# Kernel tuning notes

Hardware: AMD Instinct MI355X
Metric: run time of the kernel (lower is better)

The kernel has to match this reference:

```python
import jax, jax.numpy as jnp
import numpy as np

CACHE_LEN = 1024
EPS = 1e-5

def layer_norm(x, g, b):
    m = jnp.mean(x, axis=-1, keepdims=True)
    var = jnp.mean(jnp.square(x - m), axis=-1, keepdims=True)
    return (x - m) * jax.lax.rsqrt(var + EPS) * g + b

def setup_inputs() -> dict:
    key = jax.random.key(0)
    ks = jax.random.split(key, 16)
    B, Lq, Lk, D_IN, D_OUT = 4, 4096, 5119, 512, 512
    s = 1.0 / np.sqrt(D_IN)
    return {
        "q": jax.random.normal(ks[0], (B, Lq, D_IN), jnp.float32),
        "k": jax.random.normal(ks[1], (B, Lk, D_IN), jnp.float32),
        "v": jax.random.normal(ks[2], (B, Lk, D_IN), jnp.float32),
        "gq": jnp.ones((D_IN,), jnp.float32),
        "bq": jnp.zeros((D_IN,), jnp.float32),
        "gk": jnp.ones((D_IN,), jnp.float32),
        "bk": jnp.zeros((D_IN,), jnp.float32),
        "gv": jnp.ones((D_IN,), jnp.float32),
        "bv": jnp.zeros((D_IN,), jnp.float32),
        "Wq": jax.random.uniform(ks[3], (D_IN, D_OUT), jnp.float32, -s, s),
        "bwq": jax.random.uniform(ks[4], (D_OUT,), jnp.float32, -s, s),
        "Wk": jax.random.uniform(ks[5], (D_IN, D_OUT), jnp.float32, -s, s),
        "bwk": jax.random.uniform(ks[6], (D_OUT,), jnp.float32, -s, s),
        "Wv": jax.random.uniform(ks[7], (D_IN, D_OUT), jnp.float32, -s, s),
        "bwv": jax.random.uniform(ks[8], (D_OUT,), jnp.float32, -s, s),
    }

def reference(q, k, v, gq, bq, gk, bk, gv, bv, Wq, bwq, Wk, bwk, Wv, bwv):
    B, Lq, _ = q.shape
    Lk = k.shape[1]
    qp = layer_norm(q, gq, bq) @ Wq + bwq            # [B,Lq,Do]
    kp = layer_norm(k, gk, bk) @ Wk + bwk            # [B,Lk,Do]
    vp = layer_norm(v, gv, bv) @ Wv + bwv            # [B,Lk,Do]
    kv = jax.nn.relu(kp) * vp                         # [B,Lk,Do]
    # integrate3 skew-pad builds a banded ones mask: query row i attends to
    # kv columns [sup+i, sup+i+cache_len-1]. Equivalent sliding-window sum
    # computed via prefix sums (O(Lk*d) instead of O(Lq*Lk*d)).
    sup = Lk - Lq - CACHE_LEN + 1
    cs = jnp.cumsum(kv, axis=1)
    cs = jnp.concatenate([jnp.zeros_like(cs[:, :1]), cs], axis=1)  # [B,Lk+1,Do]
    starts = sup + jnp.arange(Lq)
    weighted = cs[:, starts + CACHE_LEN] - cs[:, starts]            # [B,Lq,Do]
    return jax.nn.relu(qp) * weighted
```

## Files before the change

kernel.cpp:

```cpp
#include <hip/hip_runtime.h>

#define B     4
#define LQ    4096
#define LK    5119
#define LKP   5120
#define D     512
#define CACHE 1024
#define MQ    (B * LQ)
#define MKP   (B * LKP)
#define NCH   160
#define TI    32

typedef float  f32x4  __attribute__((ext_vector_type(4)));
typedef __bf16 bf16x2 __attribute__((ext_vector_type(2)));
typedef __bf16 bf16x8 __attribute__((ext_vector_type(8)));

__device__ __forceinline__ void async16(void* lds, const void* g)
{
    __builtin_amdgcn_global_load_lds(
        (__attribute__((address_space(1))) void*)(g),
        (__attribute__((address_space(3))) void*)(lds),
        16, 0, 0);
}

__global__ __launch_bounds__(256) void prep_kernel(
    const float* __restrict__ q, const float* __restrict__ k,
    const float* __restrict__ v,
    const float* __restrict__ gq, const float* __restrict__ bq,
    const float* __restrict__ gk, const float* __restrict__ bk,
    const float* __restrict__ gv, const float* __restrict__ bv,
    const float* __restrict__ Wq, const float* __restrict__ Wk,
    const float* __restrict__ Wv,
    __bf16* __restrict__ qn, __bf16* __restrict__ kn, __bf16* __restrict__ vn,
    __bf16* __restrict__ wtq, __bf16* __restrict__ wtk, __bf16* __restrict__ wtv)
{
    const int z = blockIdx.y;

    if (z == 3) {
        const int idx = blockIdx.x;
        if (idx >= 384) return;
        const int zz  = idx >> 7;
        const int rem = idx & 127;
        const float* W = (zz == 0) ? Wq : (zz == 1) ? Wk : Wv;
        __bf16*     Wt = (zz == 0) ? wtq : (zz == 1) ? wtk : wtv;
        const int n  = (rem & 1) * 256 + threadIdx.x;
        const int k0 = (rem >> 1) * 8;
        bf16x8 o;
#pragma unroll
        for (int j = 0; j < 8; ++j)
            o[j] = (__bf16)W[(long)(k0 + j) * D + n];
        *reinterpret_cast<bf16x8*>(Wt + (long)n * D + k0) = o;
        return;
    }

    const float *x, *g, *bb; __bf16* o;
    if (z == 0)      { x = q; g = gq; bb = bq; o = qn; }
    else if (z == 1) { x = k; g = gk; bb = bk; o = kn; }
    else             { x = v; g = gv; bb = bv; o = vn; }

    const int rp = blockIdx.x * 8 + (threadIdx.x >> 5);
    long rin;
    if (z == 0) {
        if (rp >= MQ) return;
        rin = rp;
    } else {
        const int bch = rp / LKP;
        const int i   = rp - bch * LKP;
        if (i == LK) return;
        rin = (long)bch * LK + i;
    }

    const int c0 = (threadIdx.x & 31) * 16;
    const float* xr = x + rin * D + c0;

    float4 a[4];
#pragma unroll
    for (int j = 0; j < 4; ++j)
        a[j] = *reinterpret_cast<const float4*>(xr + j * 4);

    float s = 0.f, ss = 0.f;
#pragma unroll
    for (int j = 0; j < 4; ++j) {
        s  += a[j].x + a[j].y + a[j].z + a[j].w;
        ss += a[j].x*a[j].x + a[j].y*a[j].y + a[j].z*a[j].z + a[j].w*a[j].w;
    }
#pragma unroll
    for (int m = 1; m <= 16; m <<= 1) {
        s  += __shfl_xor(s,  m, 64);
        ss += __shfl_xor(ss, m, 64);
    }
    const float mean = s * (1.f / (float)D);
    const float var  = ss * (1.f / (float)D) - mean * mean;
    const float rs   = rsqrtf(var + 1e-5f);

    bf16x8 o0, o1;
#pragma unroll
    for (int j = 0; j < 4; ++j) {
        const float4 gv4 = *reinterpret_cast<const float4*>(g  + c0 + j * 4);
        const float4 bv4 = *reinterpret_cast<const float4*>(bb + c0 + j * 4);
        const float y0 = (a[j].x - mean) * rs * gv4.x + bv4.x;
        const float y1 = (a[j].y - mean) * rs * gv4.y + bv4.y;
        const float y2 = (a[j].z - mean) * rs * gv4.z + bv4.z;
        const float y3 = (a[j].w - mean) * rs * gv4.w + bv4.w;
        if (j < 2) {
            o0[j*4+0] = (__bf16)y0; o0[j*4+1] = (__bf16)y1;
            o0[j*4+2] = (__bf16)y2; o0[j*4+3] = (__bf16)y3;
        } else {
            o1[(j-2)*4+0] = (__bf16)y0; o1[(j-2)*4+1] = (__bf16)y1;
            o1[(j-2)*4+2] = (__bf16)y2; o1[(j-2)*4+3] = (__bf16)y3;
        }
    }
    __bf16* orow = o + (long)rp * D + c0;
    *reinterpret_cast<bf16x8*>(orow)     = o0;
    *reinterpret_cast<bf16x8*>(orow + 8) = o1;
}

__global__ __launch_bounds__(256, 2) void gemm_fused_kernel(
    const __bf16* __restrict__ qn, const __bf16* __restrict__ kn,
    const __bf16* __restrict__ vn,
    const __bf16* __restrict__ wtq, const __bf16* __restrict__ wtk,
    const __bf16* __restrict__ wtv,
    const float* __restrict__ bwq, const float* __restrict__ bwk,
    const float* __restrict__ bwv,
    __bf16* __restrict__ qpb, __bf16* __restrict__ kvb,
    float* __restrict__ Csum)
{
    __shared__ __attribute__((aligned(16))) __bf16 smem[32768];

    const int bid  = blockIdx.x;
    const int tid  = threadIdx.x;
    const int lane = tid & 63;
    const int wave = tid >> 6;
    const int quad = lane >> 4;
    const int l16  = lane & 15;
    const int wm   = wave >> 1;
    const int wn   = wave & 1;
    const int lrow = lane >> 3;
    const int lcs  = ((lane & 7) ^ lrow) * 8;

    if (bid < 640) {
        __bf16* Ks  = smem;
        __bf16* Vs  = smem + 8192;
        __bf16* WKs = smem + 16384;
        __bf16* WVs = smem + 24576;

        const int ntile = bid / 160;
        const int mtile = bid - ntile * 160;

        f32x4 acck[4][4], accv[4][4];
#pragma unroll
        for (int i = 0; i < 4; ++i)
#pragma unroll
            for (int j = 0; j < 4; ++j) {
                acck[i][j] = (f32x4){0.f, 0.f, 0.f, 0.f};
                accv[i][j] = (f32x4){0.f, 0.f, 0.f, 0.f};
            }

        const long arow0 = (long)mtile * 128;
        const long brow0 = (long)ntile * 128;

        auto stage_kv = [&](int kk) {
#pragma unroll
            for (int j = 0; j < 4; ++j) {
                const int r0  = (j * 4 + wave) * 8;
                const int row = r0 + lrow;
                async16(&Ks [r0 * 64], &kn [(arow0 + row) * D + kk + lcs]);
                async16(&Vs [r0 * 64], &vn [(arow0 + row) * D + kk + lcs]);
                async16(&WKs[r0 * 64], &wtk[(brow0 + row) * D + kk + lcs]);
                async16(&WVs[r0 * 64], &wtv[(brow0 + row) * D + kk + lcs]);
            }
        };

        stage_kv(0);
        for (int kt = 0; kt < 8; ++kt) {
            __syncthreads();

            bf16x8 fa[4][2], fb[4][2];
#pragma unroll
            for (int tm = 0; tm < 4; ++tm) {
                const int m = wm * 64 + tm * 16 + l16;
#pragma unroll
                for (int kh = 0; kh < 2; ++kh)
                    fa[tm][kh] = *reinterpret_cast<const bf16x8*>(
                        &Ks[m * 64 + (((kh * 4 + quad) ^ (m & 7)) * 8)]);
            }
#pragma unroll
            for (int tn = 0; tn < 4; ++tn) {
                const int n = wn * 64 + tn * 16 + l16;
#pragma unroll
                for (int kh = 0; kh < 2; ++kh)
                    fb[tn][kh] = *reinterpret_cast<const bf16x8*>(
                        &WKs[n * 64 + (((kh * 4 + quad) ^ (n & 7)) * 8)]);
            }
#pragma unroll
            for (int kh = 0; kh < 2; ++kh)
#pragma unroll
                for (int tm = 0; tm < 4; ++tm)
#pragma unroll
                    for (int tn = 0; tn < 4; ++tn)
                        acck[tm][tn] = __builtin_amdgcn_mfma_f32_16x16x32_bf16(
                            fa[tm][kh], fb[tn][kh], acck[tm][tn], 0, 0, 0);
#pragma unroll
            for (int tm = 0; tm < 4; ++tm) {
                const int m = wm * 64 + tm * 16 + l16;
#pragma unroll
                for (int kh = 0; kh < 2; ++kh)
                    fa[tm][kh] = *reinterpret_cast<const bf16x8*>(
                        &Vs[m * 64 + (((kh * 4 + quad) ^ (m & 7)) * 8)]);
            }
#pragma unroll
            for (int tn = 0; tn < 4; ++tn) {
                const int n = wn * 64 + tn * 16 + l16;
#pragma unroll
                for (int kh = 0; kh < 2; ++kh)
                    fb[tn][kh] = *reinterpret_cast<const bf16x8*>(
                        &WVs[n * 64 + (((kh * 4 + quad) ^ (n & 7)) * 8)]);
            }
            __syncthreads();
            if (kt < 7) stage_kv((kt + 1) * 64);
#pragma unroll
            for (int kh = 0; kh < 2; ++kh)
#pragma unroll
                for (int tm = 0; tm < 4; ++tm)
#pragma unroll
                    for (int tn = 0; tn < 4; ++tn)
                        accv[tm][tn] = __builtin_amdgcn_mfma_f32_16x16x32_bf16(
                            fa[tm][kh], fb[tn][kh], accv[tm][tn], 0, 0, 0);
        }

        float part[4][2];
#pragma unroll
        for (int tn = 0; tn < 4; ++tn) { part[tn][0] = 0.f; part[tn][1] = 0.f; }
#pragma unroll
        for (int tm = 0; tm < 4; ++tm) {
            const long row0 = arow0 + wm * 64 + tm * 16 + quad * 4;
#pragma unroll
            for (int tn = 0; tn < 4; ++tn) {
                const int col = (int)brow0 + wn * 64 + tn * 16 + l16;
                const float bkc = bwk[col];
                const float bvc = bwv[col];
#pragma unroll
                for (int r = 0; r < 4; ++r) {
                    const float kp = fmaxf(acck[tm][tn][r] + bkc, 0.f);
                    const float vp = accv[tm][tn][r] + bvc;
                    const __bf16 kb = (__bf16)(kp * vp);
                    kvb[(row0 + r) * D + col] = kb;
                    part[tn][tm >> 1] += (float)kb;
                }
            }
        }
#pragma unroll
        for (int tn = 0; tn < 4; ++tn)
#pragma unroll
            for (int th = 0; th < 2; ++th) {
                float vv = part[tn][th];
                vv += __shfl_xor(vv, 16, 64);
                vv += __shfl_xor(vv, 32, 64);
                if (quad == 0) {
                    const int fc = ((int)(arow0 >> 5)) + wm * 2 + th;
                    const int bb = fc / NCH;
                    const int cc = fc - bb * NCH;
                    const int col = (int)brow0 + wn * 64 + tn * 16 + l16;
                    Csum[((long)bb * NCH + cc) * D + col] = vv;
                }
            }
    } else {
        __bf16* As = smem;
        __bf16* Bs = smem + 8192;

        const int bidq = bid - 640;

        f32x4 acc[4][4];
#pragma unroll
        for (int i = 0; i < 4; ++i)
#pragma unroll
            for (int j = 0; j < 4; ++j)
                acc[i][j] = (f32x4){0.f, 0.f, 0.f, 0.f};

        const long arow0 = (long)(bidq & 127) * 128;
        const long brow0 = (long)(bidq >> 7) * 128;

        auto stage_q = [&](int kk) {
#pragma unroll
            for (int j = 0; j < 4; ++j) {
                const int r0  = (j * 4 + wave) * 8;
                const int row = r0 + lrow;
                async16(&As[r0 * 64], &qn [(arow0 + row) * D + kk + lcs]);
                async16(&Bs[r0 * 64], &wtq[(brow0 + row) * D + kk + lcs]);
            }
        };

        stage_q(0);
        for (int kt = 0; kt < 8; ++kt) {
            __syncthreads();

            bf16x8 af[4][2], bf[4][2];
#pragma unroll
            for (int tm = 0; tm < 4; ++tm) {
                const int m = wm * 64 + tm * 16 + l16;
#pragma unroll
                for (int kh = 0; kh < 2; ++kh)
                    af[tm][kh] = *reinterpret_cast<const bf16x8*>(
                        &As[m * 64 + (((kh * 4 + quad) ^ (m & 7)) * 8)]);
            }
#pragma unroll
            for (int tn = 0; tn < 4; ++tn) {
                const int n = wn * 64 + tn * 16 + l16;
#pragma unroll
                for (int kh = 0; kh < 2; ++kh)
                    bf[tn][kh] = *reinterpret_cast<const bf16x8*>(
                        &Bs[n * 64 + (((kh * 4 + quad) ^ (n & 7)) * 8)]);
            }
            __syncthreads();
            if (kt < 7) stage_q((kt + 1) * 64);
#pragma unroll
            for (int kh = 0; kh < 2; ++kh)
#pragma unroll
                for (int tm = 0; tm < 4; ++tm)
#pragma unroll
                    for (int tn = 0; tn < 4; ++tn)
                        acc[tm][tn] = __builtin_amdgcn_mfma_f32_16x16x32_bf16(
                            af[tm][kh], bf[tn][kh], acc[tm][tn], 0, 0, 0);
        }

#pragma unroll
        for (int tm = 0; tm < 4; ++tm) {
            const long row0 = arow0 + wm * 64 + tm * 16 + quad * 4;
#pragma unroll
            for (int tn = 0; tn < 4; ++tn) {
                const int col = (int)brow0 + wn * 64 + tn * 16 + l16;
                const float bv = bwq[col];
#pragma unroll
                for (int r = 0; r < 4; ++r)
                    qpb[(row0 + r) * D + col] =
                        (__bf16)fmaxf(acc[tm][tn][r] + bv, 0.f);
            }
        }
    }
}

__global__ __launch_bounds__(256) void window_kernel(
    const __bf16* __restrict__ kv, const float* __restrict__ Csum,
    const __bf16* __restrict__ qpb, float* __restrict__ out)
{
    const int iq   = blockIdx.x;
    const int b    = blockIdx.y;
    const int i0   = iq * TI;
    const int col2 = threadIdx.x * 2;

    const float* cs = Csum + (long)b * NCH * D + col2;
    float s0 = 0.f, s1 = 0.f;
#pragma unroll
    for (int c = 0; c < 32; ++c) {
        const float2 cv = *reinterpret_cast<const float2*>(cs + (long)(iq + c) * D);
        s0 += cv.x; s1 += cv.y;
    }

    const __bf16* kvb = kv  + (long)b * LKP * D + col2;
    const __bf16* qb  = qpb + (long)b * LQ  * D + col2;
    float*        ob  = out + (long)b * LQ  * D + col2;

#pragma unroll 8
    for (int i = i0; i < i0 + TI; ++i) {
        const bf16x2 qv = *reinterpret_cast<const bf16x2*>(qb + (long)i * D);
        *reinterpret_cast<float2*>(ob + (long)i * D) =
            make_float2((float)qv[0] * s0, (float)qv[1] * s1);
        const bf16x2 lead  = *reinterpret_cast<const bf16x2*>(kvb + (long)(i + CACHE) * D);
        const bf16x2 trail = *reinterpret_cast<const bf16x2*>(kvb + (long)i * D);
        s0 += (float)lead[0] - (float)trail[0];
        s1 += (float)lead[1] - (float)trail[1];
    }
}

extern "C" void kernel_launch(void* const* d_in, const int* in_sizes, int n_in,
                              void* d_out, int out_size, void* d_ws, size_t ws_size,
                              hipStream_t stream)
{
    const float* q   = (const float*)d_in[0];
    const float* k   = (const float*)d_in[1];
    const float* v   = (const float*)d_in[2];
    const float* gq  = (const float*)d_in[3];
    const float* bq  = (const float*)d_in[4];
    const float* gk  = (const float*)d_in[5];
    const float* bk  = (const float*)d_in[6];
    const float* gv  = (const float*)d_in[7];
    const float* bv  = (const float*)d_in[8];
    const float* Wq  = (const float*)d_in[9];
    const float* bwq = (const float*)d_in[10];
    const float* Wk  = (const float*)d_in[11];
    const float* bwk = (const float*)d_in[12];
    const float* Wv  = (const float*)d_in[13];
    const float* bwv = (const float*)d_in[14];
    float* out = (float*)d_out;

    char* ws = (char*)d_ws;
    __bf16* qn   = (__bf16*)ws;
    __bf16* kn   = qn  + (long)MQ  * D;
    __bf16* vn   = kn  + (long)MKP * D;
    __bf16* qpb  = vn  + (long)MKP * D;
    __bf16* kvb  = qpb + (long)MQ  * D;
    __bf16* wtq  = kvb + (long)MKP * D;
    __bf16* wtk  = wtq + (long)D * D;
    __bf16* wtv  = wtk + (long)D * D;
    float*  Csum = (float*)(wtv + (long)D * D);

    prep_kernel<<<dim3(2560, 4), 256, 0, stream>>>(
        q, k, v, gq, bq, gk, bk, gv, bv, Wq, Wk, Wv,
        qn, kn, vn, wtq, wtk, wtv);

    gemm_fused_kernel<<<640 + 512, 256, 0, stream>>>(
        qn, kn, vn, wtq, wtk, wtv, bwq, bwk, bwv, qpb, kvb, Csum);

    window_kernel<<<dim3(LQ / TI, B), 256, 0, stream>>>(kvb, Csum, qpb, out);
}
```

Baseline: 232.2 us.

## Persistent grid-stride layernorm prep with prefetch; double-buffer Q GEMM LDS

The prep kernel now launches 256 blocks per z and grid-strides over row groups. It keeps gamma/beta in registers and prefetches the next row group's inputs while normalizing the current one. The Q-projection GEMM branch switches to two LDS buffers, so the next k-tile's async loads are issued before the current tile is read, removing one barrier per iteration. The aim is to cut launch/tail overhead and hide load latency, at the cost of less parallelism in the memory-bound prep, which may reduce bandwidth utilization.

```diff
diff --git a/kernel.cpp b/kernel.cpp
--- a/kernel.cpp
+++ b/kernel.cpp
@@ -37,19 +37,19 @@
     const int z = blockIdx.y;
 
     if (z == 3) {
-        const int idx = blockIdx.x;
-        if (idx >= 384) return;
-        const int zz  = idx >> 7;
-        const int rem = idx & 127;
-        const float* W = (zz == 0) ? Wq : (zz == 1) ? Wk : Wv;
-        __bf16*     Wt = (zz == 0) ? wtq : (zz == 1) ? wtk : wtv;
-        const int n  = (rem & 1) * 256 + threadIdx.x;
-        const int k0 = (rem >> 1) * 8;
-        bf16x8 o;
-#pragma unroll
-        for (int j = 0; j < 8; ++j)
-            o[j] = (__bf16)W[(long)(k0 + j) * D + n];
-        *reinterpret_cast<bf16x8*>(Wt + (long)n * D + k0) = o;
+        for (int idx = blockIdx.x; idx < 384; idx += gridDim.x) {
+            const int zz  = idx >> 7;
+            const int rem = idx & 127;
+            const float* W = (zz == 0) ? Wq : (zz == 1) ? Wk : Wv;
+            __bf16*     Wt = (zz == 0) ? wtq : (zz == 1) ? wtk : wtv;
+            const int n  = (rem & 1) * 256 + threadIdx.x;
+            const int k0 = (rem >> 1) * 8;
+            bf16x8 o;
+#pragma unroll
+            for (int j = 0; j < 8; ++j)
+                o[j] = (__bf16)W[(long)(k0 + j) * D + n];
+            *reinterpret_cast<bf16x8*>(Wt + (long)n * D + k0) = o;
+        }
         return;
     }
 
@@ -58,61 +58,94 @@
     else if (z == 1) { x = k; g = gk; bb = bk; o = kn; }
     else             { x = v; g = gv; bb = bv; o = vn; }
 
-    const int rp = blockIdx.x * 8 + (threadIdx.x >> 5);
-    long rin;
-    if (z == 0) {
-        if (rp >= MQ) return;
-        rin = rp;
-    } else {
-        const int bch = rp / LKP;
-        const int i   = rp - bch * LKP;
-        if (i == LK) return;
-        rin = (long)bch * LK + i;
-    }
-
-    const int c0 = (threadIdx.x & 31) * 16;
-    const float* xr = x + rin * D + c0;
+    const int groups = (z == 0) ? (MQ / 8) : (MKP / 8);
+    const int rsub   = threadIdx.x >> 5;
+    const int c0     = (threadIdx.x & 31) * 16;
+
+    float4 gr[4], br[4];
+#pragma unroll
+    for (int j = 0; j < 4; ++j) {
+        gr[j] = *reinterpret_cast<const float4*>(g  + c0 + j * 4);
+        br[j] = *reinterpret_cast<const float4*>(bb + c0 + j * 4);
+    }
+
+    auto srcptr = [&](int gi) -> const float* {
+        const int rp = gi * 8 + rsub;
+        long rin;
+        if (z == 0) rin = rp;
+        else {
+            const int bch = rp / LKP;
+            int i = rp - bch * LKP;
+            if (i == LK) i = LK - 1;
+            rin = (long)bch * LK + i;
+        }
+        return x + rin * D + c0;
+    };
 
     float4 a[4];
-#pragma unroll
-    for (int j = 0; j < 4; ++j)
-        a[j] = *reinterpret_cast<const float4*>(xr + j * 4);
-
-    float s = 0.f, ss = 0.f;
-#pragma unroll
-    for (int j = 0; j < 4; ++j) {
-        s  += a[j].x + a[j].y + a[j].z + a[j].w;
-        ss += a[j].x*a[j].x + a[j].y*a[j].y + a[j].z*a[j].z + a[j].w*a[j].w;
-    }
-#pragma unroll
-    for (int m = 1; m <= 16; m <<= 1) {
-        s  += __shfl_xor(s,  m, 64);
-        ss += __shfl_xor(ss, m, 64);
-    }
-    const float mean = s * (1.f / (float)D);
-    const float var  = ss * (1.f / (float)D) - mean * mean;
-    const float rs   = rsqrtf(var + 1e-5f);
-
-    bf16x8 o0, o1;
-#pragma unroll
-    for (int j = 0; j < 4; ++j) {
-        const float4 gv4 = *reinterpret_cast<const float4*>(g  + c0 + j * 4);
-        const float4 bv4 = *reinterpret_cast<const float4*>(bb + c0 + j * 4);
-        const float y0 = (a[j].x - mean) * rs * gv4.x + bv4.x;
-        const float y1 = (a[j].y - mean) * rs * gv4.y + bv4.y;
-        const float y2 = (a[j].z - mean) * rs * gv4.z + bv4.z;
-        const float y3 = (a[j].w - mean) * rs * gv4.w + bv4.w;
-        if (j < 2) {
-            o0[j*4+0] = (__bf16)y0; o0[j*4+1] = (__bf16)y1;
-            o0[j*4+2] = (__bf16)y2; o0[j*4+3] = (__bf16)y3;
-        } else {
-            o1[(j-2)*4+0] = (__bf16)y0; o1[(j-2)*4+1] = (__bf16)y1;
-            o1[(j-2)*4+2] = (__bf16)y2; o1[(j-2)*4+3] = (__bf16)y3;
-        }
-    }
-    __bf16* orow = o + (long)rp * D + c0;
-    *reinterpret_cast<bf16x8*>(orow)     = o0;
-    *reinterpret_cast<bf16x8*>(orow + 8) = o1;
+    {
+        const float* p = srcptr(blockIdx.x);
+#pragma unroll
+        for (int j = 0; j < 4; ++j)
+            a[j] = *reinterpret_cast<const float4*>(p + j * 4);
+    }
+
+    for (int gi = blockIdx.x; gi < groups; gi += gridDim.x) {
+        float4 nx[4];
+        const int gn = gi + gridDim.x;
+        if (gn < groups) {
+            const float* p = srcptr(gn);
+#pragma unroll
+            for (int j = 0; j < 4; ++j)
+                nx[j] = *reinterpret_cast<const float4*>(p + j * 4);
+        }
+
+        float s = 0.f, ss = 0.f;
+#pragma unroll
+        for (int j = 0; j < 4; ++j) {
+            s  += a[j].x + a[j].y + a[j].z + a[j].w;
+            ss += a[j].x*a[j].x + a[j].y*a[j].y + a[j].z*a[j].z + a[j].w*a[j].w;
+        }
+#pragma unroll
+        for (int m = 1; m <= 16; m <<= 1) {
+            s  += __shfl_xor(s,  m, 64);
+            ss += __shfl_xor(ss, m, 64);
+        }
+        const float mean = s * (1.f / (float)D);
+        const float var  = ss * (1.f / (float)D) - mean * mean;
+        const float rs   = rsqrtf(var + 1e-5f);
+
+        bf16x8 o0, o1;
+#pragma unroll
+        for (int j = 0; j < 4; ++j) {
+            const float y0 = (a[j].x - mean) * rs * gr[j].x + br[j].x;
+            const float y1 = (a[j].y - mean) * rs * gr[j].y + br[j].y;
+            const float y2 = (a[j].z - mean) * rs * gr[j].z + br[j].z;
+            const float y3 = (a[j].w - mean) * rs * gr[j].w + br[j].w;
+            if (j < 2) {
+                o0[j*4+0] = (__bf16)y0; o0[j*4+1] = (__bf16)y1;
+                o0[j*4+2] = (__bf16)y2; o0[j*4+3] = (__bf16)y3;
+            } else {
+                o1[(j-2)*4+0] = (__bf16)y0; o1[(j-2)*4+1] = (__bf16)y1;
+                o1[(j-2)*4+2] = (__bf16)y2; o1[(j-2)*4+3] = (__bf16)y3;
+            }
+        }
+
+        const int rp = gi * 8 + rsub;
+        bool valid = true;
+        if (z != 0) {
+            const int bch = rp / LKP;
+            if (rp - bch * LKP == LK) valid = false;
+        }
+        if (valid) {
+            __bf16* orow = o + (long)rp * D + c0;
+            *reinterpret_cast<bf16x8*>(orow)     = o0;
+            *reinterpret_cast<bf16x8*>(orow + 8) = o1;
+        }
+
+#pragma unroll
+        for (int j = 0; j < 4; ++j) a[j] = nx[j];
+    }
 }
 
 __global__ __launch_bounds__(256, 2) void gemm_fused_kernel(
@@ -265,8 +298,8 @@
                 }
             }
     } else {
-        __bf16* As = smem;
-        __bf16* Bs = smem + 8192;
+        __bf16* Asb[2] = { smem,         smem + 16384 };
+        __bf16* Bsb[2] = { smem + 8192,  smem + 24576 };
 
         const int bidq = bid - 640;
 
@@ -280,19 +313,21 @@
         const long arow0 = (long)(bidq & 127) * 128;
         const long brow0 = (long)(bidq >> 7) * 128;
 
-        auto stage_q = [&](int kk) {
+        auto stage_q = [&](int kk, int p) {
 #pragma unroll
             for (int j = 0; j < 4; ++j) {
                 const int r0  = (j * 4 + wave) * 8;
                 const int row = r0 + lrow;
-                async16(&As[r0 * 64], &qn [(arow0 + row) * D + kk + lcs]);
-                async16(&Bs[r0 * 64], &wtq[(brow0 + row) * D + kk + lcs]);
+                async16(&Asb[p][r0 * 64], &qn [(arow0 + row) * D + kk + lcs]);
+                async16(&Bsb[p][r0 * 64], &wtq[(brow0 + row) * D + kk + lcs]);
             }
         };
 
-        stage_q(0);
+        stage_q(0, 0);
+        __syncthreads();
         for (int kt = 0; kt < 8; ++kt) {
-            __syncthreads();
+            const int p = kt & 1;
+            if (kt < 7) stage_q((kt + 1) * 64, p ^ 1);
 
             bf16x8 af[4][2], bf[4][2];
 #pragma unroll
@@ -301,7 +336,7 @@
 #pragma unroll
                 for (int kh = 0; kh < 2; ++kh)
                     af[tm][kh] = *reinterpret_cast<const bf16x8*>(
-                        &As[m * 64 + (((kh * 4 + quad) ^ (m & 7)) * 8)]);
+                        &Asb[p][m * 64 + (((kh * 4 + quad) ^ (m & 7)) * 8)]);
             }
 #pragma unroll
             for (int tn = 0; tn < 4; ++tn) {
@@ -309,10 +344,8 @@
 #pragma unroll
                 for (int kh = 0; kh < 2; ++kh)
                     bf[tn][kh] = *reinterpret_cast<const bf16x8*>(
-                        &Bs[n * 64 + (((kh * 4 + quad) ^ (n & 7)) * 8)]);
-            }
-            __syncthreads();
-            if (kt < 7) stage_q((kt + 1) * 64);
+                        &Bsb[p][n * 64 + (((kh * 4 + quad) ^ (n & 7)) * 8)]);
+            }
 #pragma unroll
             for (int kh = 0; kh < 2; ++kh)
 #pragma unroll
@@ -321,6 +354,7 @@
                     for (int tn = 0; tn < 4; ++tn)
                         acc[tm][tn] = __builtin_amdgcn_mfma_f32_16x16x32_bf16(
                             af[tm][kh], bf[tn][kh], acc[tm][tn], 0, 0, 0);
+            if (kt < 7) __syncthreads();
         }
 
 #pragma unroll
@@ -404,7 +438,7 @@
     __bf16* wtv  = wtk + (long)D * D;
     float*  Csum = (float*)(wtv + (long)D * D);
 
-    prep_kernel<<<dim3(2560, 4), 256, 0, stream>>>(
+    prep_kernel<<<dim3(256, 4), 256, 0, stream>>>(
         q, k, v, gq, bq, gk, bk, gv, bv, Wq, Wk, Wv,
         qn, kn, vn, wtq, wtk, wtv);
 
```

Result: no change. 230.4 us (-0.8%).
